# Kernel optimization log

Measured on AMD Instinct MI355X. Metric: run time of the kernel, lower is better.

The kernel has to match this reference:

```python
import jax, jax.numpy as jnp
import numpy as np

B, S, H, NH = 2, 2048, 1024, 16
HD = H // NH  # 64


def setup_inputs() -> dict:
    key = jax.random.key(0)
    ks = jax.random.split(key, 10)
    scale = 1.0 / np.sqrt(H)
    inp = {
        "hidden_states": jax.random.normal(ks[0], (B, S, H), dtype=jnp.float32),
        # mask: 1.0 -> masked (gets -10000 added), 0.0 -> attend
        "attention_mask": jax.random.randint(ks[1], (B, S), 0, 2).astype(jnp.float32),
        "Wq": jax.random.normal(ks[2], (H, H), dtype=jnp.float32) * scale,
        "bq": jnp.zeros((H,), dtype=jnp.float32),
        "Wk": jax.random.normal(ks[3], (H, H), dtype=jnp.float32) * scale,
        "bk": jnp.zeros((H,), dtype=jnp.float32),
        "Wv": jax.random.normal(ks[4], (H, H), dtype=jnp.float32) * scale,
        "bv": jnp.zeros((H,), dtype=jnp.float32),
        "Wo": jax.random.normal(ks[5], (H, H), dtype=jnp.float32) * scale,
        "bo": jnp.zeros((H,), dtype=jnp.float32),
    }
    return inp


def _split_heads(x):
    # [B, S, H] -> [B, NH, S, HD]
    return x.reshape(B, S, NH, HD).transpose(0, 2, 1, 3)


def reference(hidden_states, attention_mask, Wq, bq, Wk, bk, Wv, bv, Wo, bo):
    q = _split_heads(hidden_states @ Wq + bq)
    k = _split_heads(hidden_states @ Wk + bk)
    v = _split_heads(hidden_states @ Wv + bv)
    # [B, NH, S, S]
    scores = jnp.einsum("bhqd,bhkd->bhqk", q, k) / jnp.sqrt(
        jnp.asarray(HD, dtype=jnp.float32))
    # mask [B, S] -> [B, 1, 1, S]; mask==1 means masked out
    scores = scores + attention_mask[:, None, None, :] * -10000.0
    probs = jax.nn.softmax(scores, axis=-1)  # dropout = identity (eval)
    ctx = jnp.einsum("bhqk,bhkd->bhqd", probs, v)
    ctx = ctx.transpose(0, 2, 1, 3).reshape(B, S, H)
    return ctx @ Wo + bo
```

## Files before the change

kernel.cpp:

```cpp
#include <hip/hip_runtime.h>
#include <hip/hip_bf16.h>
#include <math.h>

#define NB 2
#define SS 2048
#define HH 1024
#define NHEAD 16
#define HDIM 64
#define NTOK (NB * SS)

#define QSCALE 0.18033688011112042f

typedef __attribute__((ext_vector_type(8))) short short8;
typedef __attribute__((ext_vector_type(4))) float f32x4;
typedef __attribute__((ext_vector_type(16))) float f32x16;

#define SWZ16(row, boff) ((boff) ^ (((row) & 7) << 4))

__device__ __forceinline__ unsigned short f2b(float x) {
    union { float f; unsigned int u; } v; v.f = x;
    unsigned int u = v.u + 0x7fff + ((v.u >> 16) & 1);
    return (unsigned short)(u >> 16);
}

__device__ __forceinline__ unsigned pk2a(float lo, float hi) {
    unsigned r;
    asm("v_cvt_pk_bf16_f32 %0, %1, %2" : "=v"(r) : "v"(lo), "v"(hi));
    return r;
}

__device__ __forceinline__ float exp2fast(float x) {
#if __has_builtin(__builtin_amdgcn_exp2f)
    return __builtin_amdgcn_exp2f(x);
#else
    return exp2f(x);
#endif
}

__device__ __forceinline__ void gl16(const void* g, void* l) {
    __builtin_amdgcn_global_load_lds(
        (const __attribute__((address_space(1))) void*)g,
        (__attribute__((address_space(3))) void*)l, 16, 0, 0);
}

__global__ __launch_bounds__(256) void cvt_hs(
    const float* __restrict__ X, unsigned short* __restrict__ Y)
{
    const size_t i = ((size_t)blockIdx.x * 256 + threadIdx.x) * 8;
    float4 v0 = *(const float4*)(X + i);
    float4 v1 = *(const float4*)(X + i + 4);
    short8 o;
    o[0] = f2b(v0.x); o[1] = f2b(v0.y); o[2] = f2b(v0.z); o[3] = f2b(v0.w);
    o[4] = f2b(v1.x); o[5] = f2b(v1.y); o[6] = f2b(v1.z); o[7] = f2b(v1.w);
    *(short8*)(Y + i) = o;
}

__global__ __launch_bounds__(256) void mask_scan(
    const float* __restrict__ mask, int* __restrict__ idx,
    float* __restrict__ bias, int* __restrict__ cnt)
{
    __shared__ int part[256];
    const int b = blockIdx.x;
    const int tid = threadIdx.x;

    int loc[8]; int m = 0;
    const float* mp = mask + (size_t)b * SS + tid * 8;
#pragma unroll
    for (int j = 0; j < 8; ++j) { loc[j] = (mp[j] == 0.0f) ? 1 : 0; m += loc[j]; }
    part[tid] = m;
    __syncthreads();
    for (int d = 1; d < 256; d <<= 1) {
        int v = (tid >= d) ? part[tid - d] : 0;
        __syncthreads();
        part[tid] += v;
        __syncthreads();
    }
    int base = part[tid] - m;
    const int total = part[255];
#pragma unroll
    for (int j = 0; j < 8; ++j)
        if (loc[j]) idx[(size_t)b * SS + (base++)] = tid * 8 + j;
    if (tid == 0) cnt[b] = total;
    __syncthreads();
    for (int j = tid; j < SS; j += 256) {
        if (j >= total) idx[(size_t)b * SS + j] = 0;
        bias[(size_t)b * SS + j] = (j < total) ? 0.0f : -1e30f;
    }
}

__global__ __launch_bounds__(256) void transpose_w(
    const float* __restrict__ W0, const float* __restrict__ W1,
    const float* __restrict__ W2, const float* __restrict__ W3,
    unsigned short* __restrict__ Wt)
{
    const float* W = blockIdx.z == 0 ? W0 : blockIdx.z == 1 ? W1 :
                     blockIdx.z == 2 ? W2 : W3;
    unsigned short* dst = Wt + (size_t)blockIdx.z * HH * HH;
    __shared__ unsigned short T[64][72];
    const int tid = threadIdx.x;
    const int n0 = blockIdx.x * 64, k0 = blockIdx.y * 64;
    {
        const int r = tid >> 2, c4 = (tid & 3) * 16;
        const float* src = W + (size_t)(k0 + r) * HH + n0 + c4;
#pragma unroll
        for (int j = 0; j < 16; j += 4) {
            float4 v = *(const float4*)(src + j);
            T[c4 + j + 0][r] = f2b(v.x); T[c4 + j + 1][r] = f2b(v.y);
            T[c4 + j + 2][r] = f2b(v.z); T[c4 + j + 3][r] = f2b(v.w);
        }
    }
    __syncthreads();
    {
        const int n = tid >> 2, sc = (tid & 3) * 2;
#pragma unroll
        for (int u = 0; u < 2; ++u) {
            short8 v = *(const short8*)&T[n][(sc + u) * 8];
            *(short8*)(dst + (size_t)(n0 + n) * HH + k0 + (sc + u) * 8) = v;
        }
    }
}

template<int OUT>
__global__ __launch_bounds__(256) void gemm_bf16(
    const unsigned short* __restrict__ A, const unsigned short* __restrict__ Bt,
    const float* __restrict__ b0, const float* __restrict__ b1,
    const float* __restrict__ b2, void* __restrict__ Cout)
{
    __shared__ __align__(16) unsigned short As[2][128 * 64];
    __shared__ __align__(16) unsigned short Bs[2][128 * 64];

    const int tid = threadIdx.x;
    const int w  = tid >> 6;
    const int l  = tid & 63;
    const int g  = l >> 4, c = l & 15;
    const int wr = w >> 1, wc = w & 1;
    const int m0 = blockIdx.y * 128, n0 = blockIdx.x * 128;

    const int dr = l >> 3;
    const int gc = (l & 7) ^ dr;

    const unsigned short* aBase = A  + (size_t)(m0 + w * 32 + dr) * HH + gc * 8;
    const unsigned short* bBase = Bt + (size_t)(n0 + w * 32 + dr) * HH + gc * 8;

    f32x4 acc[4][4];
#pragma unroll
    for (int mi = 0; mi < 4; ++mi)
#pragma unroll
        for (int ni = 0; ni < 4; ++ni)
            acc[mi][ni] = (f32x4){0.f, 0.f, 0.f, 0.f};

    const int swz = (c & 7) * 8;

#define STAGE(kt_, bb) {                                                      \
    const int koff = (kt_) * 64;                                              \
    _Pragma("unroll")                                                         \
    for (int i_ = 0; i_ < 4; ++i_) {                                          \
        gl16(aBase + koff + (size_t)i_ * 8 * HH, (void*)&As[bb][(w*4+i_)*512]); \
        gl16(bBase + koff + (size_t)i_ * 8 * HH, (void*)&Bs[bb][(w*4+i_)*512]); \
    } }

    STAGE(0, 0);
    STAGE(1, 1);

    for (int kt = 0; kt < 16; ++kt) {
        const int cb = kt & 1;
        if (kt < 15) asm volatile("s_waitcnt vmcnt(8)" ::: "memory");
        else         asm volatile("s_waitcnt vmcnt(0)" ::: "memory");
        __builtin_amdgcn_s_barrier();
        __builtin_amdgcn_sched_barrier(0);

        short8 af[2][4], bf[2][4];
#pragma unroll
        for (int ks = 0; ks < 2; ++ks) {
            const int kb = ks * 32;
#pragma unroll
            for (int mi = 0; mi < 4; ++mi) {
                const int row = wr * 64 + mi * 16 + c;
                af[ks][mi] = *(const short8*)&As[cb][row * 64 + ((kb + g * 8) ^ swz)];
            }
#pragma unroll
            for (int ni = 0; ni < 4; ++ni) {
                const int row = wc * 64 + ni * 16 + c;
                bf[ks][ni] = *(const short8*)&Bs[cb][row * 64 + ((kb + g * 8) ^ swz)];
            }
        }
        __builtin_amdgcn_s_setprio(1);
#pragma unroll
        for (int ks = 0; ks < 2; ++ks)
#pragma unroll
            for (int mi = 0; mi < 4; ++mi)
#pragma unroll
                for (int ni = 0; ni < 4; ++ni)
                    acc[mi][ni] = __builtin_amdgcn_mfma_f32_16x16x32_bf16(
                        af[ks][mi], bf[ks][ni], acc[mi][ni], 0, 0, 0);
        __builtin_amdgcn_s_setprio(0);

        __builtin_amdgcn_sched_barrier(0);
        __builtin_amdgcn_s_barrier();
        __builtin_amdgcn_sched_barrier(0);
        if (kt + 2 < 16) STAGE(kt + 2, cb);
    }
#undef STAGE

    if (OUT == 0) {
        const int which = n0 >> 10;
        const float* bp = which == 0 ? b0 : which == 1 ? b1 : b2;
        const float scl = which == 0 ? QSCALE : 1.0f;
        unsigned short* dst = (unsigned short*)Cout + (size_t)which * NTOK * HH;
#pragma unroll
        for (int ni = 0; ni < 4; ++ni) {
            const int nl = (n0 + wc * 64 + ni * 16 + c) & 1023;
            const int h = nl >> 6, d = nl & 63;
            const float bv = bp[nl];
#pragma unroll
            for (int mi = 0; mi < 4; ++mi) {
                const int mBase = m0 + wr * 64 + mi * 16 + g * 4;
#pragma unroll
                for (int j = 0; j < 4; ++j) {
                    const int m = mBase + j;
                    const int b = m >> 11, si = m & 2047;
                    dst[(((size_t)(b * 16 + h)) * SS + si) * 64 + d] =
                        f2b((acc[mi][ni][j] + bv) * scl);
                }
            }
        }
    } else {
#pragma unroll
        for (int ni = 0; ni < 4; ++ni) {
            const int n = n0 + wc * 64 + ni * 16 + c;
            const float bv = b0[n];
#pragma unroll
            for (int mi = 0; mi < 4; ++mi) {
                const int mBase = m0 + wr * 64 + mi * 16 + g * 4;
#pragma unroll
                for (int j = 0; j < 4; ++j)
                    ((float*)Cout)[(size_t)(mBase + j) * HH + n] =
                        acc[mi][ni][j] + bv;
            }
        }
    }
}

__global__ __launch_bounds__(256) void vtrans(
    const unsigned short* __restrict__ Vh, const int* __restrict__ idx,
    unsigned short* __restrict__ Vt)
{
    __shared__ unsigned short T[64][72];
    const int tid = threadIdx.x;
    const int bh = blockIdx.y;
    const int b  = bh >> 4;
    const int s0 = blockIdx.x * 64;
    {
        const int r = tid >> 2, dc = (tid & 3) * 16;
        const int sidx = idx[(size_t)b * SS + s0 + r];
        const unsigned short* src = Vh + ((size_t)bh * SS + sidx) * 64 + dc;
        short8 v0 = *(const short8*)src;
        short8 v1 = *(const short8*)(src + 8);
#pragma unroll
        for (int j = 0; j < 8; ++j) {
            T[dc + j][r]     = (unsigned short)v0[j];
            T[dc + 8 + j][r] = (unsigned short)v1[j];
        }
    }
    __syncthreads();
    {
        const int d = tid >> 2, sc = (tid & 3) * 2;
#pragma unroll
        for (int u = 0; u < 2; ++u) {
            short8 v = *(const short8*)&T[d][(sc + u) * 8];
            *(short8*)(Vt + ((size_t)bh * 64 + d) * SS + s0 + (sc + u) * 8) = v;
        }
    }
}

__global__ __launch_bounds__(256) void attn_mfma(
    const unsigned short* __restrict__ Qb, const unsigned short* __restrict__ Kb,
    const unsigned short* __restrict__ Vtb, const float* __restrict__ biasg,
    const int* __restrict__ idxg, const int* __restrict__ cntg,
    unsigned short* __restrict__ ctx)
{
    __shared__ __align__(16) unsigned short Ks[2][64 * 64];
    __shared__ __align__(16) unsigned short Vts[2][64 * 64];
    __shared__ float Sc[4][32];

    const int wg  = blockIdx.x;
    const int swg = (wg & 7) * 64 + (wg >> 3);
    const int qx  = swg & 15;
    const int bh  = swg >> 4;

    const int tid = threadIdx.x;
    const int l   = tid & 63;
    const int wq  = tid >> 6;
    const int hi  = l >> 5;
    const int c   = l & 31;
    const int b   = bh >> 4, h = bh & 15;
    const int q0  = qx * 128 + wq * 32;

    const unsigned short* Qp = Qb  + (size_t)bh * SS * 64;
    const unsigned short* Kp = Kb  + (size_t)bh * SS * 64;
    const unsigned short* Vp = Vtb + (size_t)bh * 64 * SS;
    const float* biasp = biasg + (size_t)b * SS;
    const int* idxb = idxg + (size_t)b * SS;

    const int cnt    = cntg[b];
    const int nt     = (cnt + 63) >> 6;
    const int ntFull = cnt >> 6;

    const int sr  = tid >> 3;
    const int sc8 = tid & 7;

    short8 qf[4];
    {
        const unsigned short* qrow = Qp + (size_t)(q0 + c) * 64 + hi * 8;
#pragma unroll
        for (int s = 0; s < 4; ++s) qf[s] = *(const short8*)(qrow + s * 16);
    }

    f32x16 oacc[2];
#pragma unroll
    for (int dt = 0; dt < 2; ++dt)
#pragma unroll
        for (int r = 0; r < 16; ++r) oacc[dt][r] = 0.f;

    float ls[4] = {0.f, 0.f, 0.f, 0.f};

    short8 kr0, kr1, vr0, vr1;

#define LOADREG(t_) {                                                         \
    const int* ip_ = idxb + (t_) * 64;                                        \
    const int sA_ = ip_[sr], sB_ = ip_[sr + 32];                              \
    kr0 = *(const short8*)(Kp + (size_t)sA_ * 64 + sc8 * 8);                  \
    kr1 = *(const short8*)(Kp + (size_t)sB_ * 64 + sc8 * 8);                  \
    vr0 = *(const short8*)(Vp + (size_t)sr * SS + (t_) * 64 + sc8 * 8);       \
    vr1 = *(const short8*)(Vp + (size_t)(sr + 32) * SS + (t_) * 64 + sc8 * 8); }

#define DSWRITE(bb) {                                                         \
    *(short8*)((char*)Ks[bb]  + sr * 128        + SWZ16(sr, sc8 * 16)) = kr0; \
    *(short8*)((char*)Ks[bb]  + (sr + 32) * 128 + SWZ16(sr + 32, sc8 * 16)) = kr1; \
    *(short8*)((char*)Vts[bb] + sr * 128        + SWZ16(sr, sc8 * 16)) = vr0; \
    *(short8*)((char*)Vts[bb] + (sr + 32) * 128 + SWZ16(sr + 32, sc8 * 16)) = vr1; }

    LOADREG(0);
    DSWRITE(0);
    __syncthreads();

    for (int t = 0; t < nt; ++t) {
        const int cb = t & 1;
        if (t + 1 < nt) LOADREG(t + 1);
        const bool needBias = (t >= ntFull);

#pragma unroll
        for (int hh = 0; hh < 2; ++hh) {
            f32x16 s4h;
#pragma unroll
            for (int r = 0; r < 16; ++r) s4h[r] = 0.f;
            const int krow = hh * 32 + c;
            __builtin_amdgcn_s_setprio(1);
#pragma unroll
            for (int ss = 0; ss < 4; ++ss) {
                short8 kf = *(const short8*)((char*)Ks[cb] + krow * 128 +
                                             SWZ16(krow, (ss * 2 + hi) * 16));
                s4h = __builtin_amdgcn_mfma_f32_32x32x16_bf16(kf, qf[ss], s4h, 0, 0, 0);
            }
            __builtin_amdgcn_s_setprio(0);

            float pvv[16];
            if (needBias) {
                f32x4 mqh[4];
#pragma unroll
                for (int tt = 0; tt < 4; ++tt)
                    mqh[tt] = *(const f32x4*)(biasp + t * 64 + (hh * 4 + tt) * 8 + hi * 4);
#pragma unroll
                for (int r = 0; r < 16; ++r)
                    pvv[r] = exp2fast(s4h[r] + mqh[r >> 2][r & 3]);
            } else {
#pragma unroll
                for (int r = 0; r < 16; ++r)
                    pvv[r] = exp2fast(s4h[r]);
            }
#pragma unroll
            for (int r = 0; r < 16; ++r) ls[r & 3] += pvv[r];

            unsigned wdh[8];
#pragma unroll
            for (int j = 0; j < 8; ++j) wdh[j] = pk2a(pvv[2 * j], pvv[2 * j + 1]);
#pragma unroll
            for (int g4 = 0; g4 < 2; ++g4) {
                asm volatile("v_permlane32_swap_b32 %0, %1"
                             : "+v"(wdh[4 * g4 + 0]), "+v"(wdh[4 * g4 + 2]));
                asm volatile("v_permlane32_swap_b32 %0, %1"
                             : "+v"(wdh[4 * g4 + 1]), "+v"(wdh[4 * g4 + 3]));
            }

            __builtin_amdgcn_s_setprio(1);
#pragma unroll
            for (int s2 = 0; s2 < 2; ++s2) {
                const int ss = hh * 2 + s2;
                union { unsigned u[4]; short8 s8; } pa;
#pragma unroll
                for (int u_ = 0; u_ < 4; ++u_) pa.u[u_] = wdh[4 * s2 + u_];
#pragma unroll
                for (int dt = 0; dt < 2; ++dt) {
                    const int vrow = dt * 32 + c;
                    short8 vf = *(const short8*)((char*)Vts[cb] + vrow * 128 +
                                                 SWZ16(vrow, (ss * 2 + hi) * 16));
                    oacc[dt] = __builtin_amdgcn_mfma_f32_32x32x16_bf16(pa.s8, vf, oacc[dt], 0, 0, 0);
                }
            }
            __builtin_amdgcn_s_setprio(0);
        }

        if (t + 1 < nt) DSWRITE(cb ^ 1);
        __syncthreads();
    }
#undef LOADREG
#undef DSWRITE

    float lsum = (ls[0] + ls[1]) + (ls[2] + ls[3]);
    lsum += __shfl_xor(lsum, 32, 64);

    Sc[wq][c] = lsum;
    asm volatile("s_waitcnt lgkmcnt(0)" ::: "memory");
    f32x4 lq[4];
#pragma unroll
    for (int tt = 0; tt < 4; ++tt)
        lq[tt] = *(const f32x4*)&Sc[wq][tt * 8 + hi * 4];

#pragma unroll
    for (int dt = 0; dt < 2; ++dt)
#pragma unroll
        for (int r = 0; r < 16; ++r) {
            const int row = (r & 3) + 8 * (r >> 2) + 4 * hi;
            const float val = oacc[dt][r] / lq[r >> 2][r & 3];
            ctx[((size_t)(b * SS + q0 + row)) * HH + h * 64 + dt * 32 + c] = f2b(val);
        }
}

extern "C" void kernel_launch(void* const* d_in, const int* in_sizes, int n_in,
                              void* d_out, int out_size, void* d_ws, size_t ws_size,
                              hipStream_t stream)
{
    const float* hs   = (const float*)d_in[0];
    const float* mask = (const float*)d_in[1];
    const float* Wq   = (const float*)d_in[2];
    const float* bq   = (const float*)d_in[3];
    const float* Wk   = (const float*)d_in[4];
    const float* bk   = (const float*)d_in[5];
    const float* Wv   = (const float*)d_in[6];
    const float* bv   = (const float*)d_in[7];
    const float* Wo   = (const float*)d_in[8];
    const float* bo   = (const float*)d_in[9];
    float* out = (float*)d_out;

    unsigned short* Ab   = (unsigned short*)d_ws;
    unsigned short* Wt   = Ab + (size_t)NTOK * HH;
    unsigned short* Qh   = Wt + (size_t)4 * HH * HH;
    unsigned short* Kh   = Qh + (size_t)NTOK * HH;
    unsigned short* Vh   = Kh + (size_t)NTOK * HH;
    unsigned short* Vt   = Vh + (size_t)NTOK * HH;
    unsigned short* ctxb = Vt + (size_t)NTOK * HH;
    float* biasb = (float*)(ctxb + (size_t)NTOK * HH);
    int*   idxb  = (int*)(biasb + (size_t)NB * SS);
    int*   cntb  = idxb + (size_t)NB * SS;

    dim3 blk(256);

    cvt_hs<<<dim3(NTOK * HH / (8 * 256)), blk, 0, stream>>>(hs, Ab);
    mask_scan<<<dim3(NB), blk, 0, stream>>>(mask, idxb, biasb, cntb);
    transpose_w<<<dim3(16, 16, 4), blk, 0, stream>>>(Wq, Wk, Wv, Wo, Wt);

    gemm_bf16<0><<<dim3(24, 32), blk, 0, stream>>>(Ab, Wt, bq, bk, bv, Qh);

    vtrans<<<dim3(SS / 64, NB * NHEAD), blk, 0, stream>>>(Vh, idxb, Vt);

    attn_mfma<<<dim3(512), blk, 0, stream>>>(Qh, Kh, Vt, biasb, idxb, cntb, ctxb);

    gemm_bf16<2><<<dim3(8, 32), blk, 0, stream>>>(ctxb, Wt + 3 * (size_t)HH * HH,
                                                  bo, bo, bo, out);
}
```

Baseline: 112.1 us.

## Merge prep kernels into one launch and retile QKV GEMM with K-step 32

Folds the hidden-state conversion, weight transpose and mask scan kernels into a single prep kernel, dispatched by block index, to cut two kernel launches. Splits the templated GEMM into separate QKV and output kernels. The QKV GEMM now stages 32-wide K tiles (32 iterations, smaller LDS buffers) with a new swizzle, which may raise occupancy but adds more barriers per tile.

```diff
diff --git a/kernel.cpp b/kernel.cpp
--- a/kernel.cpp
+++ b/kernel.cpp
@@ -43,88 +43,179 @@
         (__attribute__((address_space(3))) void*)l, 16, 0, 0);
 }
 
-__global__ __launch_bounds__(256) void cvt_hs(
-    const float* __restrict__ X, unsigned short* __restrict__ Y)
-{
-    const size_t i = ((size_t)blockIdx.x * 256 + threadIdx.x) * 8;
-    float4 v0 = *(const float4*)(X + i);
-    float4 v1 = *(const float4*)(X + i + 4);
-    short8 o;
-    o[0] = f2b(v0.x); o[1] = f2b(v0.y); o[2] = f2b(v0.z); o[3] = f2b(v0.w);
-    o[4] = f2b(v1.x); o[5] = f2b(v1.y); o[6] = f2b(v1.z); o[7] = f2b(v1.w);
-    *(short8*)(Y + i) = o;
-}
-
-__global__ __launch_bounds__(256) void mask_scan(
-    const float* __restrict__ mask, int* __restrict__ idx,
-    float* __restrict__ bias, int* __restrict__ cnt)
-{
-    __shared__ int part[256];
-    const int b = blockIdx.x;
-    const int tid = threadIdx.x;
-
-    int loc[8]; int m = 0;
-    const float* mp = mask + (size_t)b * SS + tid * 8;
-#pragma unroll
-    for (int j = 0; j < 8; ++j) { loc[j] = (mp[j] == 0.0f) ? 1 : 0; m += loc[j]; }
-    part[tid] = m;
-    __syncthreads();
-    for (int d = 1; d < 256; d <<= 1) {
-        int v = (tid >= d) ? part[tid - d] : 0;
-        __syncthreads();
-        part[tid] += v;
-        __syncthreads();
-    }
-    int base = part[tid] - m;
-    const int total = part[255];
-#pragma unroll
-    for (int j = 0; j < 8; ++j)
-        if (loc[j]) idx[(size_t)b * SS + (base++)] = tid * 8 + j;
-    if (tid == 0) cnt[b] = total;
-    __syncthreads();
-    for (int j = tid; j < SS; j += 256) {
-        if (j >= total) idx[(size_t)b * SS + j] = 0;
-        bias[(size_t)b * SS + j] = (j < total) ? 0.0f : -1e30f;
-    }
-}
-
-__global__ __launch_bounds__(256) void transpose_w(
+__global__ __launch_bounds__(256) void prep(
+    const float* __restrict__ hs,
+    const float* __restrict__ mask,
     const float* __restrict__ W0, const float* __restrict__ W1,
     const float* __restrict__ W2, const float* __restrict__ W3,
-    unsigned short* __restrict__ Wt)
+    unsigned short* __restrict__ Ab,
+    unsigned short* __restrict__ Wt,
+    int* __restrict__ idx, float* __restrict__ bias, int* __restrict__ cnt)
 {
-    const float* W = blockIdx.z == 0 ? W0 : blockIdx.z == 1 ? W1 :
-                     blockIdx.z == 2 ? W2 : W3;
-    unsigned short* dst = Wt + (size_t)blockIdx.z * HH * HH;
     __shared__ unsigned short T[64][72];
+    __shared__ int part[256];
+    const int bid = blockIdx.x;
     const int tid = threadIdx.x;
-    const int n0 = blockIdx.x * 64, k0 = blockIdx.y * 64;
-    {
-        const int r = tid >> 2, c4 = (tid & 3) * 16;
-        const float* src = W + (size_t)(k0 + r) * HH + n0 + c4;
-#pragma unroll
-        for (int j = 0; j < 16; j += 4) {
-            float4 v = *(const float4*)(src + j);
-            T[c4 + j + 0][r] = f2b(v.x); T[c4 + j + 1][r] = f2b(v.y);
-            T[c4 + j + 2][r] = f2b(v.z); T[c4 + j + 3][r] = f2b(v.w);
-        }
-    }
-    __syncthreads();
-    {
-        const int n = tid >> 2, sc = (tid & 3) * 2;
-#pragma unroll
-        for (int u = 0; u < 2; ++u) {
-            short8 v = *(const short8*)&T[n][(sc + u) * 8];
-            *(short8*)(dst + (size_t)(n0 + n) * HH + k0 + (sc + u) * 8) = v;
-        }
-    }
-}
-
-template<int OUT>
-__global__ __launch_bounds__(256) void gemm_bf16(
+
+    if (bid < 2048) {
+        const size_t i = ((size_t)bid * 256 + tid) * 8;
+        float4 v0 = *(const float4*)(hs + i);
+        float4 v1 = *(const float4*)(hs + i + 4);
+        short8 o;
+        o[0] = f2b(v0.x); o[1] = f2b(v0.y); o[2] = f2b(v0.z); o[3] = f2b(v0.w);
+        o[4] = f2b(v1.x); o[5] = f2b(v1.y); o[6] = f2b(v1.z); o[7] = f2b(v1.w);
+        *(short8*)(Ab + i) = o;
+    } else if (bid < 3072) {
+        const int t = bid - 2048;
+        const int z = t >> 8;
+        const int n0 = (t & 15) * 64, k0 = ((t >> 4) & 15) * 64;
+        const float* W = z == 0 ? W0 : z == 1 ? W1 : z == 2 ? W2 : W3;
+        unsigned short* dst = Wt + (size_t)z * HH * HH;
+        {
+            const int r = tid >> 2, c4 = (tid & 3) * 16;
+            const float* src = W + (size_t)(k0 + r) * HH + n0 + c4;
+#pragma unroll
+            for (int j = 0; j < 16; j += 4) {
+                float4 v = *(const float4*)(src + j);
+                T[c4 + j + 0][r] = f2b(v.x); T[c4 + j + 1][r] = f2b(v.y);
+                T[c4 + j + 2][r] = f2b(v.z); T[c4 + j + 3][r] = f2b(v.w);
+            }
+        }
+        __syncthreads();
+        {
+            const int n = tid >> 2, sc = (tid & 3) * 2;
+#pragma unroll
+            for (int u = 0; u < 2; ++u) {
+                short8 v = *(const short8*)&T[n][(sc + u) * 8];
+                *(short8*)(dst + (size_t)(n0 + n) * HH + k0 + (sc + u) * 8) = v;
+            }
+        }
+    } else {
+        const int b = bid - 3072;
+        int loc[8]; int m = 0;
+        const float* mp = mask + (size_t)b * SS + tid * 8;
+#pragma unroll
+        for (int j = 0; j < 8; ++j) { loc[j] = (mp[j] == 0.0f) ? 1 : 0; m += loc[j]; }
+        part[tid] = m;
+        __syncthreads();
+        for (int d = 1; d < 256; d <<= 1) {
+            int v = (tid >= d) ? part[tid - d] : 0;
+            __syncthreads();
+            part[tid] += v;
+            __syncthreads();
+        }
+        int base = part[tid] - m;
+        const int total = part[255];
+#pragma unroll
+        for (int j = 0; j < 8; ++j)
+            if (loc[j]) idx[(size_t)b * SS + (base++)] = tid * 8 + j;
+        if (tid == 0) cnt[b] = total;
+        __syncthreads();
+        for (int j = tid; j < SS; j += 256) {
+            if (j >= total) idx[(size_t)b * SS + j] = 0;
+            bias[(size_t)b * SS + j] = (j < total) ? 0.0f : -1e30f;
+        }
+    }
+}
+
+__global__ __launch_bounds__(256) void gemm_qkv(
     const unsigned short* __restrict__ A, const unsigned short* __restrict__ Bt,
     const float* __restrict__ b0, const float* __restrict__ b1,
-    const float* __restrict__ b2, void* __restrict__ Cout)
+    const float* __restrict__ b2, unsigned short* __restrict__ Cout)
+{
+    __shared__ __align__(16) unsigned short As[2][128 * 32];
+    __shared__ __align__(16) unsigned short Bs[2][128 * 32];
+
+    const int tid = threadIdx.x;
+    const int w  = tid >> 6;
+    const int l  = tid & 63;
+    const int g  = l >> 4, c = l & 15;
+    const int wr = w >> 1, wc = w & 1;
+    const int m0 = blockIdx.y * 128, n0 = blockIdx.x * 128;
+
+    const int srow = l >> 2;
+    const int gch  = (l & 3) ^ (srow & 3);
+
+    f32x4 acc[4][4];
+#pragma unroll
+    for (int mi = 0; mi < 4; ++mi)
+#pragma unroll
+        for (int ni = 0; ni < 4; ++ni)
+            acc[mi][ni] = (f32x4){0.f, 0.f, 0.f, 0.f};
+
+#define STAGE(kt_, bb) {                                                      \
+    _Pragma("unroll")                                                         \
+    for (int u_ = 0; u_ < 2; ++u_) {                                          \
+        const int rb_ = (w * 2 + u_) * 16;                                    \
+        gl16(A  + (size_t)(m0 + rb_ + srow) * HH + (kt_) * 32 + gch * 8,      \
+             (void*)&As[bb][rb_ * 32]);                                       \
+        gl16(Bt + (size_t)(n0 + rb_ + srow) * HH + (kt_) * 32 + gch * 8,      \
+             (void*)&Bs[bb][rb_ * 32]);                                       \
+    } }
+
+    STAGE(0, 0);
+    STAGE(1, 1);
+
+    for (int kt = 0; kt < 32; ++kt) {
+        const int cb = kt & 1;
+        if (kt < 31) asm volatile("s_waitcnt vmcnt(4)" ::: "memory");
+        else         asm volatile("s_waitcnt vmcnt(0)" ::: "memory");
+        __builtin_amdgcn_s_barrier();
+        __builtin_amdgcn_sched_barrier(0);
+
+        short8 af[4], bf[4];
+#pragma unroll
+        for (int mi = 0; mi < 4; ++mi) {
+            const int row = wr * 64 + mi * 16 + c;
+            af[mi] = *(const short8*)&As[cb][row * 32 + ((g * 8) ^ ((c & 3) * 8))];
+        }
+#pragma unroll
+        for (int ni = 0; ni < 4; ++ni) {
+            const int row = wc * 64 + ni * 16 + c;
+            bf[ni] = *(const short8*)&Bs[cb][row * 32 + ((g * 8) ^ ((c & 3) * 8))];
+        }
+        __builtin_amdgcn_s_setprio(1);
+#pragma unroll
+        for (int mi = 0; mi < 4; ++mi)
+#pragma unroll
+            for (int ni = 0; ni < 4; ++ni)
+                acc[mi][ni] = __builtin_amdgcn_mfma_f32_16x16x32_bf16(
+                    af[mi], bf[ni], acc[mi][ni], 0, 0, 0);
+        __builtin_amdgcn_s_setprio(0);
+
+        __builtin_amdgcn_sched_barrier(0);
+        __builtin_amdgcn_s_barrier();
+        __builtin_amdgcn_sched_barrier(0);
+        if (kt + 2 < 32) STAGE(kt + 2, cb);
+    }
+#undef STAGE
+
+    const int which = n0 >> 10;
+    const float* bp = which == 0 ? b0 : which == 1 ? b1 : b2;
+    const float scl = which == 0 ? QSCALE : 1.0f;
+    unsigned short* dst = Cout + (size_t)which * NTOK * HH;
+#pragma unroll
+    for (int ni = 0; ni < 4; ++ni) {
+        const int nl = (n0 + wc * 64 + ni * 16 + c) & 1023;
+        const int h = nl >> 6, d = nl & 63;
+        const float bv = bp[nl];
+#pragma unroll
+        for (int mi = 0; mi < 4; ++mi) {
+            const int mBase = m0 + wr * 64 + mi * 16 + g * 4;
+#pragma unroll
+            for (int j = 0; j < 4; ++j) {
+                const int m = mBase + j;
+                const int b = m >> 11, si = m & 2047;
+                dst[(((size_t)(b * 16 + h)) * SS + si) * 64 + d] =
+                    f2b((acc[mi][ni][j] + bv) * scl);
+            }
+        }
+    }
+}
+
+__global__ __launch_bounds__(256) void gemm_out(
+    const unsigned short* __restrict__ A, const unsigned short* __restrict__ Bt,
+    const float* __restrict__ b0, float* __restrict__ Cout)
 {
     __shared__ __align__(16) unsigned short As[2][128 * 64];
     __shared__ __align__(16) unsigned short Bs[2][128 * 64];
@@ -202,41 +293,16 @@
     }
 #undef STAGE
 
-    if (OUT == 0) {
-        const int which = n0 >> 10;
-        const float* bp = which == 0 ? b0 : which == 1 ? b1 : b2;
-        const float scl = which == 0 ? QSCALE : 1.0f;
-        unsigned short* dst = (unsigned short*)Cout + (size_t)which * NTOK * HH;
-#pragma unroll
-        for (int ni = 0; ni < 4; ++ni) {
-            const int nl = (n0 + wc * 64 + ni * 16 + c) & 1023;
-            const int h = nl >> 6, d = nl & 63;
-            const float bv = bp[nl];
-#pragma unroll
-            for (int mi = 0; mi < 4; ++mi) {
-                const int mBase = m0 + wr * 64 + mi * 16 + g * 4;
-#pragma unroll
-                for (int j = 0; j < 4; ++j) {
-                    const int m = mBase + j;
-                    const int b = m >> 11, si = m & 2047;
-                    dst[(((size_t)(b * 16 + h)) * SS + si) * 64 + d] =
-                        f2b((acc[mi][ni][j] + bv) * scl);
-                }
-            }
-        }
-    } else {
-#pragma unroll
-        for (int ni = 0; ni < 4; ++ni) {
-            const int n = n0 + wc * 64 + ni * 16 + c;
-            const float bv = b0[n];
-#pragma unroll
-            for (int mi = 0; mi < 4; ++mi) {
-                const int mBase = m0 + wr * 64 + mi * 16 + g * 4;
-#pragma unroll
-                for (int j = 0; j < 4; ++j)
-                    ((float*)Cout)[(size_t)(mBase + j) * HH + n] =
-                        acc[mi][ni][j] + bv;
-            }
+#pragma unroll
+    for (int ni = 0; ni < 4; ++ni) {
+        const int n = n0 + wc * 64 + ni * 16 + c;
+        const float bv = b0[n];
+#pragma unroll
+        for (int mi = 0; mi < 4; ++mi) {
+            const int mBase = m0 + wr * 64 + mi * 16 + g * 4;
+#pragma unroll
+            for (int j = 0; j < 4; ++j)
+                Cout[(size_t)(mBase + j) * HH + n] = acc[mi][ni][j] + bv;
         }
     }
 }
@@ -465,16 +531,15 @@
 
     dim3 blk(256);
 
-    cvt_hs<<<dim3(NTOK * HH / (8 * 256)), blk, 0, stream>>>(hs, Ab);
-    mask_scan<<<dim3(NB), blk, 0, stream>>>(mask, idxb, biasb, cntb);
-    transpose_w<<<dim3(16, 16, 4), blk, 0, stream>>>(Wq, Wk, Wv, Wo, Wt);
-
-    gemm_bf16<0><<<dim3(24, 32), blk, 0, stream>>>(Ab, Wt, bq, bk, bv, Qh);
+    prep<<<dim3(3074), blk, 0, stream>>>(hs, mask, Wq, Wk, Wv, Wo,
+                                         Ab, Wt, idxb, biasb, cntb);
+
+    gemm_qkv<<<dim3(24, 32), blk, 0, stream>>>(Ab, Wt, bq, bk, bv, Qh);
 
     vtrans<<<dim3(SS / 64, NB * NHEAD), blk, 0, stream>>>(Vh, idxb, Vt);
 
     attn_mfma<<<dim3(512), blk, 0, stream>>>(Qh, Kh, Vt, biasb, idxb, cntb, ctxb);
 
-    gemm_bf16<2><<<dim3(8, 32), blk, 0, stream>>>(ctxb, Wt + 3 * (size_t)HH * HH,
-                                                  bo, bo, bo, out);
-}
+    gemm_out<<<dim3(8, 32), blk, 0, stream>>>(ctxb, Wt + 3 * (size_t)HH * HH,
+                                              bo, out);
+}
```

Result: faster. 101.6 us (-9.3%).
